# Kernel tuning notes

Hardware: AMD Instinct MI355X
Metric: run time of the kernel (lower is better)

Reference implementation:

```python
import jax, jax.numpy as jnp
import numpy as np

N, E, H, EF, NG = 50000, 600000, 128, 4, 20
R_MIN, R_MAX = 0.0, 10.0

def setup_inputs() -> dict:
    key = jax.random.key(0)
    ks = jax.random.split(key, 20)
    s = lambda fi, fo: 1.0 / np.sqrt(fi)
    inp = {
        'h': jax.random.normal(ks[0], (N, H), jnp.float32),
        'x': jax.random.normal(ks[1], (N, 3), jnp.float32),
        'edge_index': jax.random.randint(ks[2], (2, E), 0, N, jnp.int32),
        'mask_ligand': jnp.ones((N,), jnp.float32),
        'edge_attr': jax.random.normal(ks[3], (E, EF), jnp.float32),
        # edge_mlp: Linear(2H+EF+NG,H) silu Linear(H,H) silu
        'We1': jax.random.normal(ks[4], (2*H+EF+NG, H), jnp.float32) * s(2*H+EF+NG, H),
        'be1': jnp.zeros((H,), jnp.float32),
        'We2': jax.random.normal(ks[5], (H, H), jnp.float32) * s(H, H),
        'be2': jnp.zeros((H,), jnp.float32),
        # edge_inf: Linear(H,1) sigmoid
        'Winf': jax.random.normal(ks[6], (H, 1), jnp.float32) * s(H, 1),
        'binf': jnp.zeros((1,), jnp.float32),
        # x_mlp: Linear(H,H) silu Linear(H,1,no bias, gain 0.001) tanh
        'Wx1': jax.random.normal(ks[7], (H, H), jnp.float32) * s(H, H),
        'bx1': jnp.zeros((H,), jnp.float32),
        'Wx2': jax.random.normal(ks[8], (H, 1), jnp.float32) * (0.001 * s(H, 1)),
        # node_mlp: Linear(2H,H) silu Linear(H,H)
        'Wn1': jax.random.normal(ks[9], (2*H, H), jnp.float32) * s(2*H, H),
        'bn1': jnp.zeros((H,), jnp.float32),
        'Wn2': jax.random.normal(ks[10], (H, H), jnp.float32) * s(H, H),
        'bn2': jnp.zeros((H,), jnp.float32),
    }
    return inp

def _gaussian_smearing(d):
    # d: [E,1] -> [E,NG]
    offset = jnp.linspace(R_MIN, R_MAX, NG, dtype=d.dtype)
    coeff = -0.5 / (offset[1] - offset[0]) ** 2
    return jnp.exp(coeff * (d - offset) ** 2)

def reference(h, x, edge_index, mask_ligand, edge_attr,
              We1, be1, We2, be2, Winf, binf, Wx1, bx1, Wx2,
              Wn1, bn1, Wn2, bn2):
    src, dst = edge_index[0], edge_index[1]
    hi, hj = h[dst], h[src]                      # [E,H]
    rel_x = x[dst] - x[src]                      # [E,3]
    d_sq = jnp.sum(rel_x ** 2, -1, keepdims=True)  # [E,1]
    d = jnp.sqrt(d_sq + 1e-8)
    d_feat = _gaussian_smearing(d)               # [E,NG]
    edge_feat = jnp.concatenate([d_feat, edge_attr], -1)
    inp = jnp.concatenate([hi, hj, edge_feat], -1)  # [E,2H+NG+EF]
    mij = jax.nn.silu(jax.nn.silu(inp @ We1 + be1) @ We2 + be2)  # [E,H]
    eij = jax.nn.sigmoid(mij @ Winf + binf)       # [E,1]
    n = h.shape[0]
    mi = jax.ops.segment_sum(mij * eij, dst, num_segments=n)  # [N,H]
    h_new = h + (jax.nn.silu(jnp.concatenate([mi, h], -1) @ Wn1 + bn1) @ Wn2 + bn2)
    gate = jnp.tanh(jax.nn.silu(mij @ Wx1 + bx1) @ Wx2)        # [E,1]
    delta_x = jax.ops.segment_sum(rel_x / (d + 1.0) * gate, dst, num_segments=n)
    x_new = x + delta_x * mask_ligand[:, None]
    return h_new, x_new
```

## Files before the change

### kernel.cpp

```cpp
#include <hip/hip_runtime.h>
#include <hip/hip_bf16.h>
#include <cstdint>

#define NN 50000
#define NE 600000
#define HD 128
#define NG 20
#define EF 4
#define K1 280
#define TILES (NE/64)
#define EGRID 512
#define ROWU 148
#define NTILE 782
#define SW(r) ((r) ^ (((r)>>3)&7))
#define EDW 12
#define TLW 520

typedef __attribute__((ext_vector_type(4))) float f32x4;
typedef __attribute__((ext_vector_type(8))) __bf16 bf16x8;
typedef __attribute__((ext_vector_type(4))) unsigned int u32x4;

__device__ __forceinline__ float fast_rcp(float x){ return __builtin_amdgcn_rcpf(x); }
__device__ __forceinline__ float silu_f(float x){ return x * fast_rcp(1.0f + __expf(-x)); }
__device__ __forceinline__ float sigmoid_f(float x){ return fast_rcp(1.0f + __expf(-x)); }
__device__ __forceinline__ float tanh_f(float x){ return 1.0f - 2.0f*fast_rcp(__expf(2.0f*x)+1.0f); }

__device__ __forceinline__ uint32_t pk2(float a, float b){
  uint32_t ua = __float_as_uint(a); ua += 0x7FFFu + ((ua>>16)&1u);
  uint32_t ub = __float_as_uint(b); ub += 0x7FFFu + ((ub>>16)&1u);
  return (ua>>16) | (ub & 0xFFFF0000u);
}
__device__ __forceinline__ uint16_t bfb(float a){
  uint32_t ua = __float_as_uint(a); ua += 0x7FFFu + ((ua>>16)&1u);
  return (uint16_t)(ua>>16);
}
__device__ __forceinline__ float bf2f(uint16_t b){ return __uint_as_float(((uint32_t)b)<<16); }
__device__ __forceinline__ f32x4 MF(u32x4 a, u32x4 b, f32x4 c){
  return __builtin_amdgcn_mfma_f32_16x16x32_bf16(
      __builtin_bit_cast(bf16x8, a), __builtin_bit_cast(bf16x8, b), c, 0, 0, 0);
}

__global__ void __launch_bounds__(256) h2bf_kernel(
    const float* __restrict__ h, uint32_t* __restrict__ hb)
{
  const size_t i = ((size_t)blockIdx.x*256 + threadIdx.x)*8;
  const float4 a = *reinterpret_cast<const float4*>(h + i);
  const float4 b = *reinterpret_cast<const float4*>(h + i + 4);
  u32x4 v = {pk2(a.x,a.y), pk2(a.z,a.w), pk2(b.x,b.y), pk2(b.z,b.w)};
  *reinterpret_cast<u32x4*>(hb + i/2) = v;
}

__global__ void __launch_bounds__(512) hist_kernel(
    const int* __restrict__ ei, int* __restrict__ cnt)
{
  const int e = blockIdx.x*512 + threadIdx.x;
  if (e < NE) atomicAdd(&cnt[ei[NE + e]], 1);
}

__global__ void __launch_bounds__(512) scanA_kernel(
    int* __restrict__ cur, int* __restrict__ bsums)
{
  __shared__ int s[512];
  const int tid = threadIdx.x;
  const int i = blockIdx.x*512 + tid;
  const int v = (i < NN) ? cur[i] : 0;
  s[tid] = v; __syncthreads();
  #pragma unroll
  for (int d = 1; d < 512; d <<= 1){
    const int t = (tid >= d) ? s[tid-d] : 0;
    __syncthreads();
    s[tid] += t;
    __syncthreads();
  }
  if (i < NN) cur[i] = s[tid] - v;
  if (tid == 511) bsums[blockIdx.x] = s[511];
}

__global__ void scanB_kernel(int* __restrict__ bsums)
{
  if (threadIdx.x == 0 && blockIdx.x == 0){
    int acc = 0;
    for (int b = 0; b < 98; ++b){ const int t = bsums[b]; bsums[b] = acc; acc += t; }
  }
}

__global__ void __launch_bounds__(512) scanC_kernel(
    int* __restrict__ cur, const int* __restrict__ bsums)
{
  const int i = blockIdx.x*512 + threadIdx.x;
  if (i < NN) cur[i] += bsums[blockIdx.x];
}

__global__ void __launch_bounds__(512) fill_kernel(
    const int* __restrict__ ei, int* __restrict__ cur, int* __restrict__ perm)
{
  const int e = blockIdx.x*512 + threadIdx.x;
  if (e < NE){
    const int p = atomicAdd(&cur[ei[NE + e]], 1);
    perm[p] = e;
  }
}

__global__ void __launch_bounds__(256) pregather_kernel(
    const int* __restrict__ ei, const float* __restrict__ x,
    const float* __restrict__ eattr, const int* __restrict__ perm,
    uint32_t* __restrict__ edata)
{
  const int i = blockIdx.x*256 + threadIdx.x;
  if (i >= NE) return;
  const int e = perm[i];
  const int sj = ei[e], dj = ei[NE + e];
  const float ax = x[dj*3+0]-x[sj*3+0];
  const float ay = x[dj*3+1]-x[sj*3+1];
  const float az = x[dj*3+2]-x[sj*3+2];
  const float dd = sqrtf(ax*ax + ay*ay + az*az + 1e-8f);
  const float4 e4 = *reinterpret_cast<const float4*>(eattr + (size_t)e*EF);
  uint32_t* dp = edata + (size_t)i*EDW;
  u32x4 v0 = {(uint32_t)sj, (uint32_t)dj, __float_as_uint(ax), __float_as_uint(ay)};
  u32x4 v1 = {__float_as_uint(az), __float_as_uint(dd), __float_as_uint(e4.x), __float_as_uint(e4.y)};
  u32x4 v2 = {__float_as_uint(e4.z), __float_as_uint(e4.w), 0u, 0u};
  *reinterpret_cast<u32x4*>(dp)     = v0;
  *reinterpret_cast<u32x4*>(dp + 4) = v1;
  *reinterpret_cast<u32x4*>(dp + 8) = v2;
}

#define EDGE_LDS_U32 (64*ROWU + 4096 + 4096 + 2*TLW + 64)
#define EDGE_LDS_B (EDGE_LDS_U32*4)

__global__ void __launch_bounds__(512, 4) edge_red_kernel(
    const uint32_t* __restrict__ hb, const uint32_t* __restrict__ edata,
    const float* __restrict__ We1, const float* __restrict__ be1,
    const float* __restrict__ We2, const float* __restrict__ be2,
    const float* __restrict__ Winf, const float* __restrict__ binf,
    const float* __restrict__ Wx1, const float* __restrict__ bx1,
    const float* __restrict__ Wx2, float* __restrict__ out)
{
  extern __shared__ uint32_t smem[];
  uint32_t* s_inp = smem;
  uint16_t* t1f   = (uint16_t*)(smem + 64*ROWU);
  uint16_t* mf_   = (uint16_t*)(smem + 64*ROWU + 4096);
  uint32_t* tlb   = smem + 64*ROWU + 8192;
  float*    s_eij = (float*)(smem + 64*ROWU + 8192 + 2*TLW);

  const int tid = threadIdx.x;
  const int w = tid >> 6, l = tid & 63;
  const int lo = l & 15, hi = l >> 4;
  const int col = w*16 + lo;
  const int r8 = tid >> 3, p8 = tid & 7;
  const int ks2 = w >> 1;
  const int lp  = ((w&1)*2 + (lo>>3))*16 + 4*hi;
  const int jj  = lo & 7;
  const int lsw = SW(l);

  u32x4 B1[9], B2[4], B3[4];
  #pragma unroll
  for (int ks = 0; ks < 9; ++ks){
    float f[8];
    #pragma unroll
    for (int j = 0; j < 8; ++j){
      const int k = ks*32 + hi*8 + j;
      f[j] = (k < K1) ? We1[k*HD + col] : 0.0f;
    }
    B1[ks] = {pk2(f[0],f[1]), pk2(f[2],f[3]), pk2(f[4],f[5]), pk2(f[6],f[7])};
  }
  #pragma unroll
  for (int ks = 0; ks < 4; ++ks){
    float f2[8], f3[8];
    #pragma unroll
    for (int j = 0; j < 8; ++j){
      const int k = ks*32 + hi*8 + j;
      f2[j] = We2[k*HD + col];
      f3[j] = Wx1[k*HD + col];
    }
    B2[ks] = {pk2(f2[0],f2[1]), pk2(f2[2],f2[3]), pk2(f2[4],f2[5]), pk2(f2[6],f2[7])};
    B3[ks] = {pk2(f3[0],f3[1]), pk2(f3[2],f3[3]), pk2(f3[4],f3[5]), pk2(f3[6],f3[7])};
  }
  const float vbe1 = be1[col], vbe2 = be2[col], vbx1 = bx1[col];
  const float wi = Winf[col], wx = Wx2[col], vbinf = binf[0];
  const float SP = 10.0f/19.0f;
  const float CO = -0.5f/(SP*SP);

  auto stage = [&](int nb, uint32_t* tq){
    {
      const uint32_t node = edata[(size_t)(nb + r8)*EDW + (p8 < 4 ? 1 : 0)];
      const uint32_t* hw = hb + (size_t)node*(HD/2) + (p8&3)*16;
      uint32_t* dp = s_inp + r8*ROWU + p8*16;
      #pragma unroll
      for (int q = 0; q < 4; ++q)
        *reinterpret_cast<u32x4*>(dp + 4*q) = *reinterpret_cast<const u32x4*>(hw + 4*q);
    }
    if (tid < 64){
      float* q_rel  = (float*)(tq);
      float* q_dist = (float*)(tq+192);
      float* q_pe   = (float*)(tq+256);
      float* q_pg   = (float*)(tq+320);
      int*   q_udst = (int*)(tq+384);
      int*   q_ust  = (int*)(tq+448);
      const uint32_t* ed = edata + (size_t)(nb + tid)*EDW;
      const u32x4 w0 = *reinterpret_cast<const u32x4*>(ed);
      const u32x4 w1 = *reinterpret_cast<const u32x4*>(ed + 4);
      const u32x4 w2 = *reinterpret_cast<const u32x4*>(ed + 8);
      const int dj   = (int)w0.y;
      const float ax = __uint_as_float(w0.z);
      const float ay = __uint_as_float(w0.w);
      const float az = __uint_as_float(w1.x);
      const float dd = __uint_as_float(w1.y);
      q_rel[3*tid+0]=ax; q_rel[3*tid+1]=ay; q_rel[3*tid+2]=az;
      q_dist[tid]=dd; q_pe[tid]=0.0f; q_pg[tid]=0.0f;
      const int dprev = __shfl_up(dj, 1);
      const int isnew = (tid == 0) || (dj != dprev);
      const unsigned long long mball = __ballot(isnew);
      const int slot = __popcll(mball << (63 - tid)) - 1;
      if (isnew){ q_udst[slot] = dj; q_ust[slot] = tid; }
      if (tid == 63){ q_ust[slot + 1] = 64; q_ust[65] = slot + 1; }
      float g[24];
      #pragma unroll
      for (int j = 0; j < 20; ++j){ const float a = dd - j*SP; g[j] = __expf(CO*a*a); }
      g[20]=__uint_as_float(w1.z); g[21]=__uint_as_float(w1.w);
      g[22]=__uint_as_float(w2.x); g[23]=__uint_as_float(w2.y);
      uint32_t* gp = s_inp + tid*ROWU + 128;
      u32x4 g0v = {pk2(g[0],g[1]),  pk2(g[2],g[3]),  pk2(g[4],g[5]),  pk2(g[6],g[7])};
      u32x4 g1v = {pk2(g[8],g[9]),  pk2(g[10],g[11]),pk2(g[12],g[13]),pk2(g[14],g[15])};
      u32x4 g2v = {pk2(g[16],g[17]),pk2(g[18],g[19]),pk2(g[20],g[21]),pk2(g[22],g[23])};
      u32x4 g3v = {0,0,0,0};
      *reinterpret_cast<u32x4*>(gp)    = g0v;
      *reinterpret_cast<u32x4*>(gp+4)  = g1v;
      *reinterpret_cast<u32x4*>(gp+8)  = g2v;
      *reinterpret_cast<u32x4*>(gp+12) = g3v;
    }
  };

  stage(blockIdx.x*64, tlb);
  __syncthreads();

  int p = 0;
  for (int t = blockIdx.x; t < TILES; t += EGRID, p ^= 1){
    uint32_t* tlp = tlb + p*TLW;
    float* s_rel  = (float*)(tlp);
    float* s_dist = (float*)(tlp+192);
    float* s_pe   = (float*)(tlp+256);
    float* s_pg   = (float*)(tlp+320);
    int*   s_udst = (int*)(tlp+384);
    int*   s_ust  = (int*)(tlp+448);

    #pragma unroll
    for (int Mt = 0; Mt < 4; ++Mt){
      const uint32_t* arow = s_inp + (Mt*16 + lo)*ROWU + hi*4;
      f32x4 acc = {0,0,0,0};
      #pragma unroll
      for (int ks = 0; ks < 9; ++ks)
        acc = MF(*reinterpret_cast<const u32x4*>(arow + ks*16), B1[ks], acc);
      #pragma unroll
      for (int reg = 0; reg < 4; ++reg)
        t1f[((Mt*4 + ks2)*64 + SW(lp+reg))*8 + jj] = bfb(silu_f(acc[reg] + vbe1));
    }
    __syncthreads();

    if (t + EGRID < TILES) stage((t + EGRID)*64, tlb + (p^1)*TLW);

    #pragma unroll
    for (int Mt = 0; Mt < 4; ++Mt){
      f32x4 acc = {0,0,0,0};
      #pragma unroll
      for (int ks = 0; ks < 4; ++ks)
        acc = MF(*reinterpret_cast<const u32x4*>(t1f + ((Mt*4+ks)*64 + lsw)*8), B2[ks], acc);
      float pq[4];
      #pragma unroll
      for (int reg = 0; reg < 4; ++reg){
        const float m = silu_f(acc[reg] + vbe2);
        mf_[((Mt*4 + ks2)*64 + SW(lp+reg))*8 + jj] = bfb(m);
        pq[reg] = m * wi;
      }
      #pragma unroll
      for (int msk = 1; msk < 16; msk <<= 1){
        #pragma unroll
        for (int reg = 0; reg < 4; ++reg) pq[reg] += __shfl_xor(pq[reg], msk);
      }
      if (lo == 0){
        #pragma unroll
        for (int reg = 0; reg < 4; ++reg) atomicAdd(&s_pe[Mt*16 + 4*hi + reg], pq[reg]);
      }
    }
    __syncthreads();

    s_eij[l] = sigmoid_f(s_pe[l] + vbinf);
    const int U = s_ust[65];

    for (int idx = tid; idx < U*HD; idx += 512){
      const int u = idx >> 7, c = idx & 127;
      const int r0 = s_ust[u], r1 = s_ust[u+1];
      const int cb = c >> 5, cc = ((c>>4)&1)*2 + ((c>>3)&1);
      const int base = (cb*64 + cc*16)*8 + (c & 7);
      const int x2 = cc*2;
      float acc = 0.0f;
      for (int r = r0; r < r1; ++r){
        const int mix = (r>>4)*2048 + base + (((r&15) ^ ((x2 + ((r>>3)&1))&7))<<3);
        acc += bf2f(mf_[mix]) * s_eij[r];
      }
      atomicAdd(out + (size_t)s_udst[u]*HD + c, acc);
    }
    #pragma unroll
    for (int Mt = 0; Mt < 4; ++Mt){
      f32x4 acc = {0,0,0,0};
      #pragma unroll
      for (int ks = 0; ks < 4; ++ks)
        acc = MF(*reinterpret_cast<const u32x4*>(mf_ + ((Mt*4+ks)*64 + lsw)*8), B3[ks], acc);
      float pq[4];
      #pragma unroll
      for (int reg = 0; reg < 4; ++reg)
        pq[reg] = silu_f(acc[reg] + vbx1) * wx;
      #pragma unroll
      for (int msk = 1; msk < 16; msk <<= 1){
        #pragma unroll
        for (int reg = 0; reg < 4; ++reg) pq[reg] += __shfl_xor(pq[reg], msk);
      }
      if (lo == 0){
        #pragma unroll
        for (int reg = 0; reg < 4; ++reg) atomicAdd(&s_pg[Mt*16 + 4*hi + reg], pq[reg]);
      }
    }
    __syncthreads();

    if (tid < 64){
      s_eij[tid] = tanh_f(s_pg[tid]) * fast_rcp(s_dist[tid] + 1.0f);
      for (int idx = tid; idx < U*3; idx += 64){
        const int u = idx/3, cc2 = idx - 3*u;
        float acc = 0.0f;
        for (int r = s_ust[u]; r < s_ust[u+1]; ++r)
          acc += s_rel[3*r+cc2] * s_eij[r];
        atomicAdd(out + (size_t)NN*HD + (size_t)s_udst[u]*3 + cc2, acc);
      }
    }
  }
}

#define FB_LDS_U32 (64*ROWU + 4096 + 4096 + 448)
#define FB_LDS_B (FB_LDS_U32*4)

__global__ void __launch_bounds__(512, 4) edge_fb_kernel(
    const float* __restrict__ h, const float* __restrict__ x,
    const int* __restrict__ ei, const float* __restrict__ eattr,
    const float* __restrict__ We1, const float* __restrict__ be1,
    const float* __restrict__ We2, const float* __restrict__ be2,
    const float* __restrict__ Winf, const float* __restrict__ binf,
    const float* __restrict__ Wx1, const float* __restrict__ bx1,
    const float* __restrict__ Wx2, float* __restrict__ out)
{
  extern __shared__ uint32_t smem[];
  uint32_t* s_inp = smem;
  uint16_t* t1f   = (uint16_t*)(smem + 64*ROWU);
  uint16_t* mf_   = (uint16_t*)(smem + 64*ROWU + 4096);
  uint32_t* tl    = smem + 64*ROWU + 8192;
  int*   s_dst  = (int*)tl;
  float* s_rel  = (float*)(tl+64);
  float* s_dist = (float*)(tl+256);
  float* s_pe   = (float*)(tl+320);
  float* s_pg   = (float*)(tl+384);

  const int tid = threadIdx.x;
  const int w = tid >> 6, l = tid & 63;
  const int lo = l & 15, hi = l >> 4;
  const int col = w*16 + lo;
  const int r8 = tid >> 3, p8 = tid & 7;
  const int ks2 = w >> 1;
  const int lp  = ((w&1)*2 + (lo>>3))*16 + 4*hi;
  const int jj  = lo & 7;
  const int lsw = SW(l);

  u32x4 B1[9], B2[4], B3[4];
  #pragma unroll
  for (int ks = 0; ks < 9; ++ks){
    float f[8];
    #pragma unroll
    for (int j = 0; j < 8; ++j){
      const int k = ks*32 + hi*8 + j;
      f[j] = (k < K1) ? We1[k*HD + col] : 0.0f;
    }
    B1[ks] = {pk2(f[0],f[1]), pk2(f[2],f[3]), pk2(f[4],f[5]), pk2(f[6],f[7])};
  }
  #pragma unroll
  for (int ks = 0; ks < 4; ++ks){
    float f2[8], f3[8];
    #pragma unroll
    for (int j = 0; j < 8; ++j){
      const int k = ks*32 + hi*8 + j;
      f2[j] = We2[k*HD + col];
      f3[j] = Wx1[k*HD + col];
    }
    B2[ks] = {pk2(f2[0],f2[1]), pk2(f2[2],f2[3]), pk2(f2[4],f2[5]), pk2(f2[6],f2[7])};
    B3[ks] = {pk2(f3[0],f3[1]), pk2(f3[2],f3[3]), pk2(f3[4],f3[5]), pk2(f3[6],f3[7])};
  }
  const float vbe1 = be1[col], vbe2 = be2[col], vbx1 = bx1[col];
  const float wi = Winf[col], wx = Wx2[col], vbinf = binf[0];
  const float SP = 10.0f/19.0f;
  const float CO = -0.5f/(SP*SP);

  for (int t = blockIdx.x; t < TILES; t += EGRID){
    const int ebase = t*64;
    __syncthreads();
    if (tid < 64){
      const int sj = ei[ebase+tid], dj = ei[NE+ebase+tid];
      const float ax = x[dj*3+0]-x[sj*3+0];
      const float ay = x[dj*3+1]-x[sj*3+1];
      const float az = x[dj*3+2]-x[sj*3+2];
      const float dd = sqrtf(ax*ax + ay*ay + az*az + 1e-8f);
      s_dst[tid] = dj;
      s_rel[3*tid+0]=ax; s_rel[3*tid+1]=ay; s_rel[3*tid+2]=az;
      s_dist[tid]=dd; s_pe[tid]=0.0f; s_pg[tid]=0.0f;
      float g[24];
      #pragma unroll
      for (int j = 0; j < 20; ++j){ const float a = dd - j*SP; g[j] = __expf(CO*a*a); }
      const float4 e4 = *reinterpret_cast<const float4*>(eattr + (size_t)(ebase+tid)*EF);
      g[20]=e4.x; g[21]=e4.y; g[22]=e4.z; g[23]=e4.w;
      uint32_t* gp = s_inp + tid*ROWU + 128;
      u32x4 g0v = {pk2(g[0],g[1]),  pk2(g[2],g[3]),  pk2(g[4],g[5]),  pk2(g[6],g[7])};
      u32x4 g1v = {pk2(g[8],g[9]),  pk2(g[10],g[11]),pk2(g[12],g[13]),pk2(g[14],g[15])};
      u32x4 g2v = {pk2(g[16],g[17]),pk2(g[18],g[19]),pk2(g[20],g[21]),pk2(g[22],g[23])};
      u32x4 g3v = {0,0,0,0};
      *reinterpret_cast<u32x4*>(gp)    = g0v;
      *reinterpret_cast<u32x4*>(gp+4)  = g1v;
      *reinterpret_cast<u32x4*>(gp+8)  = g2v;
      *reinterpret_cast<u32x4*>(gp+12) = g3v;
    }
    {
      const int e = ebase + r8;
      const int node = (p8 < 4) ? ei[NE + e] : ei[e];
      const float* hp = h + (size_t)node*HD + (p8&3)*32;
      uint32_t* dp = s_inp + r8*ROWU + p8*16;
      #pragma unroll
      for (int q = 0; q < 4; ++q){
        const float4 va = *reinterpret_cast<const float4*>(hp + 8*q);
        const float4 vb = *reinterpret_cast<const float4*>(hp + 8*q + 4);
        u32x4 v = { pk2(va.x,va.y), pk2(va.z,va.w), pk2(vb.x,vb.y), pk2(vb.z,vb.w) };
        *reinterpret_cast<u32x4*>(dp + 4*q) = v;
      }
    }
    __syncthreads();

    #pragma unroll
    for (int Mt = 0; Mt < 4; ++Mt){
      const uint32_t* arow = s_inp + (Mt*16 + lo)*ROWU + hi*4;
      f32x4 acc = {0,0,0,0};
      #pragma unroll
      for (int ks = 0; ks < 9; ++ks)
        acc = MF(*reinterpret_cast<const u32x4*>(arow + ks*16), B1[ks], acc);
      #pragma unroll
      for (int reg = 0; reg < 4; ++reg)
        t1f[((Mt*4 + ks2)*64 + SW(lp+reg))*8 + jj] = bfb(silu_f(acc[reg] + vbe1));
    }
    __syncthreads();

    #pragma unroll
    for (int Mt = 0; Mt < 4; ++Mt){
      f32x4 acc = {0,0,0,0};
      #pragma unroll
      for (int ks = 0; ks < 4; ++ks)
        acc = MF(*reinterpret_cast<const u32x4*>(t1f + ((Mt*4+ks)*64 + lsw)*8), B2[ks], acc);
      float pq[4];
      #pragma unroll
      for (int reg = 0; reg < 4; ++reg){
        const float m = silu_f(acc[reg] + vbe2);
        mf_[((Mt*4 + ks2)*64 + SW(lp+reg))*8 + jj] = bfb(m);
        pq[reg] = m * wi;
      }
      #pragma unroll
      for (int msk = 1; msk < 16; msk <<= 1){
        #pragma unroll
        for (int reg = 0; reg < 4; ++reg) pq[reg] += __shfl_xor(pq[reg], msk);
      }
      if (lo == 0){
        #pragma unroll
        for (int reg = 0; reg < 4; ++reg) atomicAdd(&s_pe[Mt*16 + 4*hi + reg], pq[reg]);
      }
    }
    __syncthreads();

    #pragma unroll
    for (int Mt = 0; Mt < 4; ++Mt){
      #pragma unroll
      for (int reg = 0; reg < 4; ++reg){
        const int r = Mt*16 + 4*hi + reg;
        const float eij = sigmoid_f(s_pe[r] + vbinf);
        const float m = bf2f(mf_[((Mt*4 + ks2)*64 + SW(lp+reg))*8 + jj]);
        atomicAdd(out + (size_t)s_dst[r]*HD + col, m*eij);
      }
    }
    #pragma unroll
    for (int Mt = 0; Mt < 4; ++Mt){
      f32x4 acc = {0,0,0,0};
      #pragma unroll
      for (int ks = 0; ks < 4; ++ks)
        acc = MF(*reinterpret_cast<const u32x4*>(mf_ + ((Mt*4+ks)*64 + lsw)*8), B3[ks], acc);
      float pq[4];
      #pragma unroll
      for (int reg = 0; reg < 4; ++reg)
        pq[reg] = silu_f(acc[reg] + vbx1) * wx;
      #pragma unroll
      for (int msk = 1; msk < 16; msk <<= 1){
        #pragma unroll
        for (int reg = 0; reg < 4; ++reg) pq[reg] += __shfl_xor(pq[reg], msk);
      }
      if (lo == 0){
        #pragma unroll
        for (int reg = 0; reg < 4; ++reg) atomicAdd(&s_pg[Mt*16 + 4*hi + reg], pq[reg]);
      }
    }
    __syncthreads();

    if (tid < 192){
      const int er = tid/3, c = tid - 3*er;
      const float gate = tanh_f(s_pg[er]);
      const float sc = gate * fast_rcp(s_dist[er] + 1.0f);
      atomicAdd(out + (size_t)NN*HD + (size_t)s_dst[er]*3 + c, s_rel[3*er+c]*sc);
    }
  }
}

#define CROW 132

__global__ void __launch_bounds__(512, 4) node_kernel(
    const float* __restrict__ h, const float* __restrict__ x,
    const float* __restrict__ mask,
    const float* __restrict__ Wn1, const float* __restrict__ bn1,
    const float* __restrict__ Wn2, const float* __restrict__ bn2,
    float* __restrict__ out)
{
  __shared__ uint32_t s_cat[64*CROW];
  __shared__ __align__(16) uint16_t t1n[4*4*64*8];

  const int tid = threadIdx.x;
  const int w = tid >> 6, l = tid & 63;
  const int lo = l & 15, hi = l >> 4;
  const int col = w*16 + lo;

  u32x4 Bn1[8], Bn2[4];
  #pragma unroll
  for (int ks = 0; ks < 8; ++ks){
    float f[8];
    #pragma unroll
    for (int j = 0; j < 8; ++j) f[j] = Wn1[(ks*32 + hi*8 + j)*HD + col];
    Bn1[ks] = {pk2(f[0],f[1]), pk2(f[2],f[3]), pk2(f[4],f[5]), pk2(f[6],f[7])};
  }
  #pragma unroll
  for (int ks = 0; ks < 4; ++ks){
    float f[8];
    #pragma unroll
    for (int j = 0; j < 8; ++j) f[j] = Wn2[(ks*32 + hi*8 + j)*HD + col];
    Bn2[ks] = {pk2(f[0],f[1]), pk2(f[2],f[3]), pk2(f[4],f[5]), pk2(f[6],f[7])};
  }
  const float vbn1 = bn1[col], vbn2 = bn2[col];
  const int nbase = blockIdx.x*64;
  const int ks2 = w >> 1;
  const int lp  = ((w&1)*2 + (lo>>3))*16 + 4*hi;
  const int jj  = lo & 7;

  {
    const int r = tid >> 3, p = tid & 7;
    const int n = nbase + r;
    uint32_t* dp = s_cat + r*CROW + p*16;
    if (n < NN){
      const float* sp = (p < 4) ? (out + (size_t)n*HD + p*32)
                                : (h   + (size_t)n*HD + (p-4)*32);
      #pragma unroll
      for (int q = 0; q < 8; ++q){
        const float4 v = *reinterpret_cast<const float4*>(sp + 4*q);
        dp[2*q]   = pk2(v.x, v.y);
        dp[2*q+1] = pk2(v.z, v.w);
      }
    } else {
      #pragma unroll
      for (int q = 0; q < 16; ++q) dp[q] = 0u;
    }
  }
  __syncthreads();

  #pragma unroll
  for (int Mt = 0; Mt < 4; ++Mt){
    const uint32_t* arow = s_cat + (Mt*16 + lo)*CROW + hi*4;
    f32x4 acc = {0,0,0,0};
    #pragma unroll
    for (int ks = 0; ks < 8; ++ks)
      acc = MF(*reinterpret_cast<const u32x4*>(arow + ks*16), Bn1[ks], acc);
    uint16_t* tp = t1n + ((Mt*4 + ks2)*64 + lp)*8 + jj;
    #pragma unroll
    for (int reg = 0; reg < 4; ++reg)
      tp[reg*8] = bfb(silu_f(acc[reg] + vbn1));
  }
  __syncthreads();

  #pragma unroll
  for (int Mt = 0; Mt < 4; ++Mt){
    f32x4 acc = {0,0,0,0};
    #pragma unroll
    for (int ks = 0; ks < 4; ++ks)
      acc = MF(*reinterpret_cast<const u32x4*>(t1n + ((Mt*4+ks)*64 + l)*8), Bn2[ks], acc);
    #pragma unroll
    for (int reg = 0; reg < 4; ++reg){
      const int n = nbase + Mt*16 + 4*hi + reg;
      if (n < NN)
        out[(size_t)n*HD + col] = h[(size_t)n*HD + col] + acc[reg] + vbn2;
    }
  }

  if (tid < 192){
    const int r = tid/3, c = tid - 3*r;
    const int n = nbase + r;
    if (n < NN){
      const size_t ix = (size_t)NN*HD + (size_t)n*3 + c;
      out[ix] = x[(size_t)n*3 + c] + out[ix]*mask[n];
    }
  }
}

extern "C" void kernel_launch(void* const* d_in, const int* in_sizes, int n_in,
                              void* d_out, int out_size, void* d_ws, size_t ws_size,
                              hipStream_t stream) {
  (void)in_sizes; (void)n_in;
  const float* h    = (const float*)d_in[0];
  const float* x    = (const float*)d_in[1];
  const int*   ei   = (const int*)  d_in[2];
  const float* mask = (const float*)d_in[3];
  const float* ea   = (const float*)d_in[4];
  const float* We1  = (const float*)d_in[5];
  const float* be1  = (const float*)d_in[6];
  const float* We2  = (const float*)d_in[7];
  const float* be2  = (const float*)d_in[8];
  const float* Winf = (const float*)d_in[9];
  const float* binf = (const float*)d_in[10];
  const float* Wx1  = (const float*)d_in[11];
  const float* bx1  = (const float*)d_in[12];
  const float* Wx2  = (const float*)d_in[13];
  const float* Wn1  = (const float*)d_in[14];
  const float* bn1  = (const float*)d_in[15];
  const float* Wn2  = (const float*)d_in[16];
  const float* bn2  = (const float*)d_in[17];
  float* out = (float*)d_out;

  uint32_t* hb    = (uint32_t*)d_ws;
  int* cursor     = (int*)d_ws + 3200000;
  int* perm       = (int*)d_ws + 3250000;
  int* bsums      = (int*)d_ws + 3850000;
  uint32_t* edata = (uint32_t*)d_ws + 3850128;
  const size_t need = (size_t)(3850128 + (size_t)NE*EDW) * 4;
  const bool use_red = ws_size >= need;

  hipFuncSetAttribute(reinterpret_cast<const void*>(edge_red_kernel),
                      hipFuncAttributeMaxDynamicSharedMemorySize, EDGE_LDS_B);
  hipFuncSetAttribute(reinterpret_cast<const void*>(edge_fb_kernel),
                      hipFuncAttributeMaxDynamicSharedMemorySize, FB_LDS_B);

  hipMemsetAsync(d_out, 0, (size_t)out_size * sizeof(float), stream);

  if (use_red){
    hipMemsetAsync(cursor, 0, (size_t)NN*4, stream);
    h2bf_kernel<<<3125, 256, 0, stream>>>(h, hb);
    hist_kernel<<<1172, 512, 0, stream>>>(ei, cursor);
    scanA_kernel<<<98, 512, 0, stream>>>(cursor, bsums);
    scanB_kernel<<<1, 64, 0, stream>>>(bsums);
    scanC_kernel<<<98, 512, 0, stream>>>(cursor, bsums);
    fill_kernel<<<1172, 512, 0, stream>>>(ei, cursor, perm);
    pregather_kernel<<<2344, 256, 0, stream>>>(ei, x, ea, perm, edata);
    edge_red_kernel<<<EGRID, 512, EDGE_LDS_B, stream>>>(
        hb, edata, We1, be1, We2, be2, Winf, binf, Wx1, bx1, Wx2, out);
  } else {
    edge_fb_kernel<<<EGRID, 512, FB_LDS_B, stream>>>(
        h, x, ei, ea, We1, be1, We2, be2, Winf, binf, Wx1, bx1, Wx2, out);
  }
  node_kernel<<<NTILE, 512, 0, stream>>>(
      h, x, mask, Wn1, bn1, Wn2, bn2, out);
}
```

Baseline: 454.3 us.

## Fuse preprocessing kernels and restructure segment reduction into fixed 16-row chunks

Merges the bf16 conversion with the destination histogram, folds the block-sum scan into the add pass, and merges the permutation fill with the pregather so each edge record is written straight to its sorted slot. This drops the perm array and several launches. In the edge kernel, each thread now reduces a fixed 16-row chunk and flushes an atomic whenever the per-row segment slot changes, instead of looping over unique destinations with variable row ranges. This removes load imbalance and the U-dependent loop, at the cost of more atomics when a segment crosses chunk boundaries. The in-segment order of edges becomes nondeterministic.

```diff
diff --git a/kernel.cpp b/kernel.cpp
--- a/kernel.cpp
+++ b/kernel.cpp
@@ -14,7 +14,7 @@
 #define NTILE 782
 #define SW(r) ((r) ^ (((r)>>3)&7))
 #define EDW 12
-#define TLW 520
+#define TLW 584
 
 typedef __attribute__((ext_vector_type(4))) float f32x4;
 typedef __attribute__((ext_vector_type(8))) __bf16 bf16x8;
@@ -40,21 +40,19 @@
       __builtin_bit_cast(bf16x8, a), __builtin_bit_cast(bf16x8, b), c, 0, 0, 0);
 }
 
-__global__ void __launch_bounds__(256) h2bf_kernel(
-    const float* __restrict__ h, uint32_t* __restrict__ hb)
-{
-  const size_t i = ((size_t)blockIdx.x*256 + threadIdx.x)*8;
-  const float4 a = *reinterpret_cast<const float4*>(h + i);
-  const float4 b = *reinterpret_cast<const float4*>(h + i + 4);
-  u32x4 v = {pk2(a.x,a.y), pk2(a.z,a.w), pk2(b.x,b.y), pk2(b.z,b.w)};
-  *reinterpret_cast<u32x4*>(hb + i/2) = v;
-}
-
-__global__ void __launch_bounds__(512) hist_kernel(
+__global__ void __launch_bounds__(512) h2bf_hist_kernel(
+    const float* __restrict__ h, uint32_t* __restrict__ hb,
     const int* __restrict__ ei, int* __restrict__ cnt)
 {
-  const int e = blockIdx.x*512 + threadIdx.x;
-  if (e < NE) atomicAdd(&cnt[ei[NE + e]], 1);
+  const int gid = blockIdx.x*512 + threadIdx.x;
+  if (gid < 800000){
+    const size_t i = (size_t)gid*8;
+    const float4 a = *reinterpret_cast<const float4*>(h + i);
+    const float4 b = *reinterpret_cast<const float4*>(h + i + 4);
+    u32x4 v = {pk2(a.x,a.y), pk2(a.z,a.w), pk2(b.x,b.y), pk2(b.z,b.w)};
+    *reinterpret_cast<u32x4*>(hb + i/2) = v;
+  }
+  if (gid < NE) atomicAdd(&cnt[ei[NE + gid]], 1);
 }
 
 __global__ void __launch_bounds__(512) scanA_kernel(
@@ -76,46 +74,35 @@
   if (tid == 511) bsums[blockIdx.x] = s[511];
 }
 
-__global__ void scanB_kernel(int* __restrict__ bsums)
-{
-  if (threadIdx.x == 0 && blockIdx.x == 0){
-    int acc = 0;
-    for (int b = 0; b < 98; ++b){ const int t = bsums[b]; bsums[b] = acc; acc += t; }
-  }
-}
-
-__global__ void __launch_bounds__(512) scanC_kernel(
+__global__ void __launch_bounds__(512) scanBC_kernel(
     int* __restrict__ cur, const int* __restrict__ bsums)
 {
+  __shared__ int pre;
+  if (threadIdx.x == 0){
+    int acc = 0;
+    for (int b = 0; b < (int)blockIdx.x; ++b) acc += bsums[b];
+    pre = acc;
+  }
+  __syncthreads();
   const int i = blockIdx.x*512 + threadIdx.x;
-  if (i < NN) cur[i] += bsums[blockIdx.x];
-}
-
-__global__ void __launch_bounds__(512) fill_kernel(
-    const int* __restrict__ ei, int* __restrict__ cur, int* __restrict__ perm)
-{
-  const int e = blockIdx.x*512 + threadIdx.x;
-  if (e < NE){
-    const int p = atomicAdd(&cur[ei[NE + e]], 1);
-    perm[p] = e;
-  }
-}
-
-__global__ void __launch_bounds__(256) pregather_kernel(
+  if (i < NN) cur[i] += pre;
+}
+
+__global__ void __launch_bounds__(256) fillpg_kernel(
     const int* __restrict__ ei, const float* __restrict__ x,
-    const float* __restrict__ eattr, const int* __restrict__ perm,
+    const float* __restrict__ eattr, int* __restrict__ cur,
     uint32_t* __restrict__ edata)
 {
-  const int i = blockIdx.x*256 + threadIdx.x;
-  if (i >= NE) return;
-  const int e = perm[i];
+  const int e = blockIdx.x*256 + threadIdx.x;
+  if (e >= NE) return;
   const int sj = ei[e], dj = ei[NE + e];
+  const int p = atomicAdd(&cur[dj], 1);
   const float ax = x[dj*3+0]-x[sj*3+0];
   const float ay = x[dj*3+1]-x[sj*3+1];
   const float az = x[dj*3+2]-x[sj*3+2];
   const float dd = sqrtf(ax*ax + ay*ay + az*az + 1e-8f);
   const float4 e4 = *reinterpret_cast<const float4*>(eattr + (size_t)e*EF);
-  uint32_t* dp = edata + (size_t)i*EDW;
+  uint32_t* dp = edata + (size_t)p*EDW;
   u32x4 v0 = {(uint32_t)sj, (uint32_t)dj, __float_as_uint(ax), __float_as_uint(ay)};
   u32x4 v1 = {__float_as_uint(az), __float_as_uint(dd), __float_as_uint(e4.x), __float_as_uint(e4.y)};
   u32x4 v2 = {__float_as_uint(e4.z), __float_as_uint(e4.w), 0u, 0u};
@@ -196,6 +183,7 @@
       float* q_pg   = (float*)(tq+320);
       int*   q_udst = (int*)(tq+384);
       int*   q_ust  = (int*)(tq+448);
+      int*   q_slot = (int*)(tq+514);
       const uint32_t* ed = edata + (size_t)(nb + tid)*EDW;
       const u32x4 w0 = *reinterpret_cast<const u32x4*>(ed);
       const u32x4 w1 = *reinterpret_cast<const u32x4*>(ed + 4);
@@ -211,6 +199,7 @@
       const int isnew = (tid == 0) || (dj != dprev);
       const unsigned long long mball = __ballot(isnew);
       const int slot = __popcll(mball << (63 - tid)) - 1;
+      q_slot[tid] = slot;
       if (isnew){ q_udst[slot] = dj; q_ust[slot] = tid; }
       if (tid == 63){ q_ust[slot + 1] = 64; q_ust[65] = slot + 1; }
       float g[24];
@@ -242,6 +231,7 @@
     float* s_pg   = (float*)(tlp+320);
     int*   s_udst = (int*)(tlp+384);
     int*   s_ust  = (int*)(tlp+448);
+    int*   s_slot = (int*)(tlp+514);
 
     #pragma unroll
     for (int Mt = 0; Mt < 4; ++Mt){
@@ -284,20 +274,26 @@
     __syncthreads();
 
     s_eij[l] = sigmoid_f(s_pe[l] + vbinf);
-    const int U = s_ust[65];
-
-    for (int idx = tid; idx < U*HD; idx += 512){
-      const int u = idx >> 7, c = idx & 127;
-      const int r0 = s_ust[u], r1 = s_ust[u+1];
+
+    {
+      const int rb16 = (tid >> 7) << 4;
+      const int c    = tid & 127;
       const int cb = c >> 5, cc = ((c>>4)&1)*2 + ((c>>3)&1);
-      const int base = (cb*64 + cc*16)*8 + (c & 7);
+      const int base = (rb16 >> 4)*2048 + (cb*64 + cc*16)*8 + (c & 7);
       const int x2 = cc*2;
       float acc = 0.0f;
-      for (int r = r0; r < r1; ++r){
-        const int mix = (r>>4)*2048 + base + (((r&15) ^ ((x2 + ((r>>3)&1))&7))<<3);
-        acc += bf2f(mf_[mix]) * s_eij[r];
-      }
-      atomicAdd(out + (size_t)s_udst[u]*HD + c, acc);
+      int sprev = s_slot[rb16];
+      #pragma unroll
+      for (int i = 0; i < 16; ++i){
+        const int s = s_slot[rb16 + i];
+        if (s != sprev){
+          atomicAdd(out + (size_t)s_udst[sprev]*HD + c, acc);
+          acc = 0.0f; sprev = s;
+        }
+        const int mix = base + ((i ^ ((x2 + (i>>3))&7)) << 3);
+        acc += bf2f(mf_[mix]) * s_eij[rb16 + i];
+      }
+      atomicAdd(out + (size_t)s_udst[sprev]*HD + c, acc);
     }
     #pragma unroll
     for (int Mt = 0; Mt < 4; ++Mt){
@@ -322,6 +318,7 @@
     __syncthreads();
 
     if (tid < 64){
+      const int U = s_ust[65];
       s_eij[tid] = tanh_f(s_pg[tid]) * fast_rcp(s_dist[tid] + 1.0f);
       for (int idx = tid; idx < U*3; idx += 64){
         const int u = idx/3, cc2 = idx - 3*u;
@@ -555,12 +552,12 @@
   const int jj  = lo & 7;
 
   {
-    const int r = tid >> 3, p = tid & 7;
+    const int r = tid >> 3, pp = tid & 7;
     const int n = nbase + r;
-    uint32_t* dp = s_cat + r*CROW + p*16;
+    uint32_t* dp = s_cat + r*CROW + pp*16;
     if (n < NN){
-      const float* sp = (p < 4) ? (out + (size_t)n*HD + p*32)
-                                : (h   + (size_t)n*HD + (p-4)*32);
+      const float* sp = (pp < 4) ? (out + (size_t)n*HD + pp*32)
+                                 : (h   + (size_t)n*HD + (pp-4)*32);
       #pragma unroll
       for (int q = 0; q < 8; ++q){
         const float4 v = *reinterpret_cast<const float4*>(sp + 4*q);
@@ -638,10 +635,9 @@
 
   uint32_t* hb    = (uint32_t*)d_ws;
   int* cursor     = (int*)d_ws + 3200000;
-  int* perm       = (int*)d_ws + 3250000;
-  int* bsums      = (int*)d_ws + 3850000;
-  uint32_t* edata = (uint32_t*)d_ws + 3850128;
-  const size_t need = (size_t)(3850128 + (size_t)NE*EDW) * 4;
+  int* bsums      = (int*)d_ws + 3250000;
+  uint32_t* edata = (uint32_t*)d_ws + 3250128;
+  const size_t need = (size_t)(3250128 + (size_t)NE*EDW) * 4;
   const bool use_red = ws_size >= need;
 
   hipFuncSetAttribute(reinterpret_cast<const void*>(edge_red_kernel),
@@ -653,13 +649,10 @@
 
   if (use_red){
     hipMemsetAsync(cursor, 0, (size_t)NN*4, stream);
-    h2bf_kernel<<<3125, 256, 0, stream>>>(h, hb);
-    hist_kernel<<<1172, 512, 0, stream>>>(ei, cursor);
+    h2bf_hist_kernel<<<1563, 512, 0, stream>>>(h, hb, ei, cursor);
     scanA_kernel<<<98, 512, 0, stream>>>(cursor, bsums);
-    scanB_kernel<<<1, 64, 0, stream>>>(bsums);
-    scanC_kernel<<<98, 512, 0, stream>>>(cursor, bsums);
-    fill_kernel<<<1172, 512, 0, stream>>>(ei, cursor, perm);
-    pregather_kernel<<<2344, 256, 0, stream>>>(ei, x, ea, perm, edata);
+    scanBC_kernel<<<98, 512, 0, stream>>>(cursor, bsums);
+    fillpg_kernel<<<2344, 256, 0, stream>>>(ei, x, ea, cursor, edata);
     edge_red_kernel<<<EGRID, 512, EDGE_LDS_B, stream>>>(
         hb, edata, We1, be1, We2, be2, Winf, binf, Wx1, bx1, Wx2, out);
   } else {
```

Measured after the change: 428.6 us, median of 2. -5.6%, faster.
